# Performance work log

Measured on AMD Instinct MI355X. Metric: run time of the kernel, lower is better.

## Reference

```python
import jax, jax.numpy as jnp
import numpy as np

N_NODES = 100000
N_EDGES = 1600000
IN_CH = 128
HID = 64
OUT = 10
N_GRAPHS = 64


def gcn_conv(x, W, b, row, col, n):
    # PyG GCNConv: xw = x @ W; add self-loops (weight 1);
    # deg = scatter_add(weight, col); norm = d^-1/2[row] * d^-1/2[col];
    # out[col] += norm * xw[row]; out += b
    xw = x @ W  # [N, out_ch]
    loop = jnp.arange(n, dtype=row.dtype)
    r = jnp.concatenate([row, loop])
    c = jnp.concatenate([col, loop])
    deg = jax.ops.segment_sum(jnp.ones_like(c, dtype=xw.dtype), c, num_segments=n)
    dis = jnp.where(deg > 0, jax.lax.rsqrt(deg), 0.0)
    norm = dis[r] * dis[c]  # [E+N]
    msgs = norm[:, None] * xw[r]  # gather + scale
    agg = jax.ops.segment_sum(msgs, c, num_segments=n)  # scatter-add
    return agg + b


def global_mean_pool(x, batch, num_graphs):
    sums = jax.ops.segment_sum(x, batch, num_segments=num_graphs)
    cnt = jax.ops.segment_sum(jnp.ones((x.shape[0],), x.dtype), batch, num_segments=num_graphs)
    return sums / jnp.maximum(cnt, 1.0)[:, None]


def setup_inputs() -> dict:
    key = jax.random.key(0)
    ks = jax.random.split(key, 9)
    x = jax.random.normal(ks[0], (N_NODES, IN_CH), dtype=jnp.float32)
    edge_index = jax.random.randint(ks[1], (2, N_EDGES), 0, N_NODES, dtype=jnp.int64)
    batch = jnp.sort(jax.random.randint(ks[2], (N_NODES,), 0, N_GRAPHS, dtype=jnp.int64))
    def glorot(k, shape):
        lim = np.sqrt(6.0 / (shape[0] + shape[1]))
        return jax.random.uniform(k, shape, jnp.float32, -lim, lim)
    W1 = glorot(ks[3], (IN_CH, HID)); b1 = jnp.zeros((HID,), jnp.float32)
    W2 = glorot(ks[4], (HID, HID)); b2 = jnp.zeros((HID,), jnp.float32)
    Wl = glorot(ks[5], (HID, OUT)); bl = jnp.zeros((OUT,), jnp.float32)
    return {"x": x, "W1": W1, "b1": b1, "W2": W2, "b2": b2,
            "Wl": Wl, "bl": bl, "edge_index": edge_index, "batch": batch}


def reference(x, W1, b1, W2, b2, Wl, bl, edge_index, batch):
    row, col = edge_index[0], edge_index[1]
    n = x.shape[0]
    h = jax.nn.relu(gcn_conv(x, W1, b1, row, col, n))
    h = jax.nn.relu(gcn_conv(h, W2, b2, row, col, n))
    g = global_mean_pool(h, batch, N_GRAPHS)  # [G, HID]
    return g @ Wl + bl  # [G, OUT]
```

## Files before the change

### kernel.cpp

```cpp
#include <hip/hip_runtime.h>


static __device__ inline ushort f32_to_bf16_rne(float f) {
    uint32_t u = __float_as_uint(f);
    uint32_t r = (u + 0x7fffu + ((u >> 16) & 1u)) >> 16;
    return (ushort)r;
}

__global__ __launch_bounds__(256) void deg_kernel(const int* __restrict__ col,
                                                  int* __restrict__ deg, int E) {
    int e = blockIdx.x * 256 + threadIdx.x;
    if (e < E) atomicAdd(&deg[col[e]], 1);
}

__global__ __launch_bounds__(256) void dis_kernel(const int* __restrict__ deg,
                                                  float* __restrict__ dis, int n) {
    int i = blockIdx.x * 256 + threadIdx.x;
    if (i < n) dis[i] = rsqrtf((float)deg[i] + 1.0f);
}

__global__ __launch_bounds__(512) void block_sum_kernel(const int* __restrict__ deg,
                                                        int* __restrict__ bsums, int n) {
    __shared__ int sm[512];
    int i = blockIdx.x * 512 + threadIdx.x;
    sm[threadIdx.x] = (i < n) ? deg[i] : 0;
    __syncthreads();
    for (int s = 256; s > 0; s >>= 1) {
        if (threadIdx.x < s) sm[threadIdx.x] += sm[threadIdx.x + s];
        __syncthreads();
    }
    if (threadIdx.x == 0) bsums[blockIdx.x] = sm[0];
}

__global__ __launch_bounds__(256) void scan_bsums_kernel(int* __restrict__ bsums, int nb) {
    __shared__ int sm[256];
    int v = (threadIdx.x < nb) ? bsums[threadIdx.x] : 0;
    sm[threadIdx.x] = v;
    __syncthreads();
    for (int off = 1; off < 256; off <<= 1) {
        int t = (threadIdx.x >= off) ? sm[threadIdx.x - off] : 0;
        __syncthreads();
        sm[threadIdx.x] += t;
        __syncthreads();
    }
    if (threadIdx.x < nb) bsums[threadIdx.x] = sm[threadIdx.x] - v;
}

__global__ __launch_bounds__(512) void scan_write_kernel(const int* __restrict__ deg,
                                                         const int* __restrict__ bsums,
                                                         int* __restrict__ rowptr,
                                                         int n, int E) {
    __shared__ int sm[512];
    int i = blockIdx.x * 512 + threadIdx.x;
    int v = (i < n) ? deg[i] : 0;
    sm[threadIdx.x] = v;
    __syncthreads();
    for (int off = 1; off < 512; off <<= 1) {
        int t = (threadIdx.x >= off) ? sm[threadIdx.x - off] : 0;
        __syncthreads();
        sm[threadIdx.x] += t;
        __syncthreads();
    }
    if (i < n) rowptr[i] = bsums[blockIdx.x] + sm[threadIdx.x] - v;
    if (blockIdx.x == 0 && threadIdx.x == 0) rowptr[n] = E;
}

__global__ __launch_bounds__(256) void fill_csr_kernel(const int* __restrict__ row,
                                                       const int* __restrict__ col,
                                                       const float* __restrict__ dis,
                                                       const int* __restrict__ rowptr,
                                                       int* __restrict__ fill,
                                                       int2* __restrict__ csr, int E) {
    int e = blockIdx.x * 256 + threadIdx.x;
    if (e >= E) return;
    int r = row[e], c = col[e];
    int pos = rowptr[c] + atomicAdd(&fill[c], 1);
    csr[pos] = make_int2(r, __float_as_int(dis[r] * dis[c]));
}

template <int K>
__global__ __launch_bounds__(256) void gemm_tiled(const float* __restrict__ x,
                                                  const float* __restrict__ W,
                                                  ushort* __restrict__ out, int n) {
    __shared__ float As[32][64];
    __shared__ float Ws[32 * 64];
    const int tid = threadIdx.x;
    const int tr = tid >> 4;
    const int tc = tid & 15;
    const int base = blockIdx.x * 64;

    float acc[4][4];
#pragma unroll
    for (int i = 0; i < 4; ++i)
#pragma unroll
        for (int j = 0; j < 4; ++j) acc[i][j] = 0.0f;

    const int tnode = tid >> 3;
    const int tk4 = (tid & 7) * 4;

    for (int kc = 0; kc < K; kc += 32) {
        __syncthreads();
#pragma unroll
        for (int h = 0; h < 2; ++h) {
            int m = tnode + h * 32;
            int node = base + m;
            float4 v = make_float4(0.f, 0.f, 0.f, 0.f);
            if (node < n) v = *(const float4*)&x[(size_t)node * K + kc + tk4];
            As[tk4 + 0][m] = v.x; As[tk4 + 1][m] = v.y;
            As[tk4 + 2][m] = v.z; As[tk4 + 3][m] = v.w;
        }
#pragma unroll
        for (int r = 0; r < 2; ++r) {
            int o = tid * 4 + r * 1024;
            *(float4*)&Ws[o] = *(const float4*)&W[kc * 64 + o];
        }
        __syncthreads();
#pragma unroll
        for (int k = 0; k < 32; ++k) {
            float4 a = *(const float4*)&As[k][tr * 4];
            float4 b = *(const float4*)&Ws[k * 64 + tc * 4];
            const float av[4] = {a.x, a.y, a.z, a.w};
            const float bv[4] = {b.x, b.y, b.z, b.w};
#pragma unroll
            for (int i = 0; i < 4; ++i)
#pragma unroll
                for (int j = 0; j < 4; ++j)
                    acc[i][j] = fmaf(av[i], bv[j], acc[i][j]);
        }
    }
#pragma unroll
    for (int i = 0; i < 4; ++i) {
        int node = base + tr * 4 + i;
        if (node < n) {
            ushort4 st;
            st.x = f32_to_bf16_rne(acc[i][0]);
            st.y = f32_to_bf16_rne(acc[i][1]);
            st.z = f32_to_bf16_rne(acc[i][2]);
            st.w = f32_to_bf16_rne(acc[i][3]);
            *(ushort4*)&out[(size_t)node * 64 + tc * 4] = st;
        }
    }
}

template <int OUT_BF16>
__global__ __launch_bounds__(256) void gcn_pull_kernel(const ushort* __restrict__ xw,
                                                       const int2* __restrict__ csr,
                                                       const int* __restrict__ rowptr,
                                                       const float* __restrict__ dis,
                                                       const float* __restrict__ b,
                                                       void* __restrict__ outv, int n) {
    const int lane = threadIdx.x & 63;
    const int wid = threadIdx.x >> 6;
    const int half = lane >> 5;
    const int q = lane & 31;
    const float2 bb = ((const float2*)b)[q];

    for (int i = blockIdx.x * 4 + wid; i < n; i += gridDim.x * 4) {
        int s = rowptr[i], t = rowptr[i + 1];
        float ax = 0.0f, ay = 0.0f;
        if (half == 0) {
            float di = dis[i];
            uint32_t u = *(const uint32_t*)(xw + ((size_t)i << 6) + (q << 1));
            float w = di * di;
            ax = w * __uint_as_float(u << 16);
            ay = w * __uint_as_float(u & 0xffff0000u);
        }
        int e = s + half;
        for (; e + 2 < t; e += 4) {
            int2 p0 = csr[e];
            int2 p1 = csr[e + 2];
            uint32_t u0 = *(const uint32_t*)(xw + ((size_t)p0.x << 6) + (q << 1));
            uint32_t u1 = *(const uint32_t*)(xw + ((size_t)p1.x << 6) + (q << 1));
            float n0 = __int_as_float(p0.y), n1 = __int_as_float(p1.y);
            ax = fmaf(n0, __uint_as_float(u0 << 16), ax);
            ay = fmaf(n0, __uint_as_float(u0 & 0xffff0000u), ay);
            ax = fmaf(n1, __uint_as_float(u1 << 16), ax);
            ay = fmaf(n1, __uint_as_float(u1 & 0xffff0000u), ay);
        }
        for (; e < t; e += 2) {
            int2 p = csr[e];
            uint32_t u = *(const uint32_t*)(xw + ((size_t)p.x << 6) + (q << 1));
            float nr = __int_as_float(p.y);
            ax = fmaf(nr, __uint_as_float(u << 16), ax);
            ay = fmaf(nr, __uint_as_float(u & 0xffff0000u), ay);
        }
        ax += __shfl_xor(ax, 32);
        ay += __shfl_xor(ay, 32);
        if (half == 0) {
            float v0 = fmaxf(ax + bb.x, 0.0f);
            float v1 = fmaxf(ay + bb.y, 0.0f);
            if (OUT_BF16) {
                ushort2 st = make_ushort2(f32_to_bf16_rne(v0), f32_to_bf16_rne(v1));
                *(ushort2*)((ushort*)outv + ((size_t)i << 6) + (q << 1)) = st;
            } else {
                *(float2*)((float*)outv + ((size_t)i << 6) + (q << 1)) = make_float2(v0, v1);
            }
        }
    }
}

__global__ __launch_bounds__(256) void pool_kernel(const ushort* __restrict__ h,
                                                   const int* __restrict__ batch,
                                                   float* __restrict__ pool,
                                                   float* __restrict__ cnt, int n) {
    const int lane = threadIdx.x & 63;
    const int wid = threadIdx.x >> 6;
    const int start = (blockIdx.x * 4 + wid) * 256;
    const int end = min(start + 256, n);
    if (start >= end) return;
    int gcur = batch[start];
    float acc = 0.0f;
    int c = 0;
    for (int i = start; i < end; ++i) {
        int g = batch[i];
        if (g != gcur) {
            atomicAdd(&pool[gcur * 64 + lane], acc);
            if (lane == 0) atomicAdd(&cnt[gcur], (float)c);
            acc = 0.0f; c = 0; gcur = g;
        }
        acc += __uint_as_float((uint32_t)h[(size_t)i * 64 + lane] << 16);
        ++c;
    }
    atomicAdd(&pool[gcur * 64 + lane], acc);
    if (lane == 0) atomicAdd(&cnt[gcur], (float)c);
}

__global__ __launch_bounds__(640) void final_kernel(const float* __restrict__ pool,
                                                    const float* __restrict__ cnt,
                                                    const float* __restrict__ Wl,
                                                    const float* __restrict__ bl,
                                                    float* __restrict__ out) {
    int tid = threadIdx.x;
    int g = tid / 10, o = tid % 10;
    float inv = 1.0f / fmaxf(cnt[g], 1.0f);
    float acc = 0.0f;
#pragma unroll
    for (int l = 0; l < 64; ++l)
        acc = fmaf(pool[g * 64 + l] * inv, Wl[l * 10 + o], acc);
    out[tid] = acc + bl[o];
}

extern "C" void kernel_launch(void* const* d_in, const int* in_sizes, int n_in,
                              void* d_out, int out_size, void* d_ws, size_t ws_size,
                              hipStream_t stream) {
    const float* x  = (const float*)d_in[0];
    const float* W1 = (const float*)d_in[1];
    const float* b1 = (const float*)d_in[2];
    const float* W2 = (const float*)d_in[3];
    const float* b2 = (const float*)d_in[4];
    const float* Wl = (const float*)d_in[5];
    const float* bl = (const float*)d_in[6];
    const int*   ei = (const int*)d_in[7];
    const int*   batch = (const int*)d_in[8];
    float* out = (float*)d_out;

    const int n = in_sizes[8];
    const int E = in_sizes[7] / 2;
    const int F = 64;

    const int* row = ei;
    const int* col = ei + E;

    char* p = (char*)d_ws;
    auto alloc = [&](size_t bytes) {
        char* r = p;
        p += (bytes + 255) & ~(size_t)255;
        return r;
    };
    int*    degi   = (int*)   alloc((size_t)n * 4);
    int*    rowptr = (int*)   alloc((size_t)(n + 1) * 4);
    int*    bsums  = (int*)   alloc(256 * 4);
    float*  dis    = (float*) alloc((size_t)n * 4);
    int2*   csr    = (int2*)  alloc((size_t)E * 8);
    ushort* xwB    = (ushort*)alloc((size_t)n * F * 2);
    float*  B      = (float*) alloc((size_t)n * F * 4);
    float*  pool   = (float*) alloc(64 * 64 * 4);
    float*  cnt    = (float*) alloc(64 * 4);

    const int nb_edge = (E + 255) / 256;
    const int nb_node = (n + 255) / 256;
    const int nb_scan = (n + 511) / 512;
    const int nb_gemm = (n + 63) / 64;

    hipMemsetAsync(degi, 0, (size_t)n * 4, stream);
    deg_kernel<<<nb_edge, 256, 0, stream>>>(col, degi, E);
    block_sum_kernel<<<nb_scan, 512, 0, stream>>>(degi, bsums, n);
    scan_bsums_kernel<<<1, 256, 0, stream>>>(bsums, nb_scan);
    scan_write_kernel<<<nb_scan, 512, 0, stream>>>(degi, bsums, rowptr, n, E);
    dis_kernel<<<nb_node, 256, 0, stream>>>(degi, dis, n);
    hipMemsetAsync(degi, 0, (size_t)n * 4, stream);
    fill_csr_kernel<<<nb_edge, 256, 0, stream>>>(row, col, dis, rowptr, degi, csr, E);

    gemm_tiled<128><<<nb_gemm, 256, 0, stream>>>(x, W1, xwB, n);
    gcn_pull_kernel<0><<<2048, 256, 0, stream>>>(xwB, csr, rowptr, dis, b1, B, n);

    gemm_tiled<64><<<nb_gemm, 256, 0, stream>>>(B, W2, xwB, n);
    gcn_pull_kernel<1><<<2048, 256, 0, stream>>>(xwB, csr, rowptr, dis, b2, B, n);

    hipMemsetAsync(pool, 0, (64 * 64 + 64) * sizeof(float), stream);
    pool_kernel<<<(n + 1023) / 1024, 256, 0, stream>>>((const ushort*)B, batch, pool, cnt, n);
    final_kernel<<<1, 640, 0, stream>>>(pool, cnt, Wl, bl, out);
}
```

Measured before the change: 496.9 us.

## Fuse CSR fill with first GEMM, drop per-edge norm, fold dis into scan

Merges the dis computation into the scan-write kernel and runs the CSR fill and the first GEMM as disjoint block ranges of one launch, so the two can overlap. The CSR now stores only source indices (halving its size), and the pull kernel gathers dis[src] per edge and applies dis[dst] once at the end. The pull loop is unrolled to four edges per half-wave, and the pool kernel uses smaller chunks per wave for more parallelism. The trade is an extra random 4-byte gather per edge in exchange for less CSR traffic and fewer launches.

Measured after the change: 436.7 us. 12.1% less time.

```diff
diff --git a/kernel.cpp b/kernel.cpp
--- a/kernel.cpp
+++ b/kernel.cpp
@@ -6,17 +6,13 @@
     uint32_t r = (u + 0x7fffu + ((u >> 16) & 1u)) >> 16;
     return (ushort)r;
 }
+static __device__ inline float bf_lo(uint32_t u) { return __uint_as_float(u << 16); }
+static __device__ inline float bf_hi(uint32_t u) { return __uint_as_float(u & 0xffff0000u); }
 
 __global__ __launch_bounds__(256) void deg_kernel(const int* __restrict__ col,
                                                   int* __restrict__ deg, int E) {
     int e = blockIdx.x * 256 + threadIdx.x;
     if (e < E) atomicAdd(&deg[col[e]], 1);
-}
-
-__global__ __launch_bounds__(256) void dis_kernel(const int* __restrict__ deg,
-                                                  float* __restrict__ dis, int n) {
-    int i = blockIdx.x * 256 + threadIdx.x;
-    if (i < n) dis[i] = rsqrtf((float)deg[i] + 1.0f);
 }
 
 __global__ __launch_bounds__(512) void block_sum_kernel(const int* __restrict__ deg,
@@ -49,6 +45,7 @@
 __global__ __launch_bounds__(512) void scan_write_kernel(const int* __restrict__ deg,
                                                          const int* __restrict__ bsums,
                                                          int* __restrict__ rowptr,
+                                                         float* __restrict__ dis,
                                                          int n, int E) {
     __shared__ int sm[512];
     int i = blockIdx.x * 512 + threadIdx.x;
@@ -61,33 +58,23 @@
         sm[threadIdx.x] += t;
         __syncthreads();
     }
-    if (i < n) rowptr[i] = bsums[blockIdx.x] + sm[threadIdx.x] - v;
+    if (i < n) {
+        rowptr[i] = bsums[blockIdx.x] + sm[threadIdx.x] - v;
+        dis[i] = rsqrtf((float)v + 1.0f);
+    }
     if (blockIdx.x == 0 && threadIdx.x == 0) rowptr[n] = E;
 }
 
-__global__ __launch_bounds__(256) void fill_csr_kernel(const int* __restrict__ row,
-                                                       const int* __restrict__ col,
-                                                       const float* __restrict__ dis,
-                                                       const int* __restrict__ rowptr,
-                                                       int* __restrict__ fill,
-                                                       int2* __restrict__ csr, int E) {
-    int e = blockIdx.x * 256 + threadIdx.x;
-    if (e >= E) return;
-    int r = row[e], c = col[e];
-    int pos = rowptr[c] + atomicAdd(&fill[c], 1);
-    csr[pos] = make_int2(r, __float_as_int(dis[r] * dis[c]));
-}
-
 template <int K>
-__global__ __launch_bounds__(256) void gemm_tiled(const float* __restrict__ x,
-                                                  const float* __restrict__ W,
-                                                  ushort* __restrict__ out, int n) {
+__device__ __forceinline__ void gemm_tile_body(const float* __restrict__ x,
+                                               const float* __restrict__ W,
+                                               ushort* __restrict__ out, int n, int bx) {
     __shared__ float As[32][64];
     __shared__ float Ws[32 * 64];
     const int tid = threadIdx.x;
     const int tr = tid >> 4;
     const int tc = tid & 15;
-    const int base = blockIdx.x * 64;
+    const int base = bx * 64;
 
     float acc[4][4];
 #pragma unroll
@@ -142,9 +129,35 @@
     }
 }
 
+template <int K>
+__global__ __launch_bounds__(256) void gemm_tiled(const float* __restrict__ x,
+                                                  const float* __restrict__ W,
+                                                  ushort* __restrict__ out, int n) {
+    gemm_tile_body<K>(x, W, out, n, blockIdx.x);
+}
+
+template <int K>
+__global__ __launch_bounds__(256) void fused_fill_gemm(
+        const float* __restrict__ x, const float* __restrict__ W,
+        ushort* __restrict__ out, int n, int nb_fill,
+        const int* __restrict__ row, const int* __restrict__ col,
+        const int* __restrict__ rowptr, int* __restrict__ fill,
+        int* __restrict__ csrs, int E) {
+    if ((int)blockIdx.x >= nb_fill) {
+        gemm_tile_body<K>(x, W, out, n, blockIdx.x - nb_fill);
+        return;
+    }
+    const int stride = nb_fill * 256;
+    for (int e = blockIdx.x * 256 + threadIdx.x; e < E; e += stride) {
+        int r = row[e], c = col[e];
+        int pos = rowptr[c] + atomicAdd(&fill[c], 1);
+        csrs[pos] = r;
+    }
+}
+
 template <int OUT_BF16>
 __global__ __launch_bounds__(256) void gcn_pull_kernel(const ushort* __restrict__ xw,
-                                                       const int2* __restrict__ csr,
+                                                       const int* __restrict__ csrs,
                                                        const int* __restrict__ rowptr,
                                                        const float* __restrict__ dis,
                                                        const float* __restrict__ b,
@@ -157,38 +170,45 @@
 
     for (int i = blockIdx.x * 4 + wid; i < n; i += gridDim.x * 4) {
         int s = rowptr[i], t = rowptr[i + 1];
+        float di = dis[i];
         float ax = 0.0f, ay = 0.0f;
         if (half == 0) {
-            float di = dis[i];
             uint32_t u = *(const uint32_t*)(xw + ((size_t)i << 6) + (q << 1));
-            float w = di * di;
-            ax = w * __uint_as_float(u << 16);
-            ay = w * __uint_as_float(u & 0xffff0000u);
+            ax = di * bf_lo(u);
+            ay = di * bf_hi(u);
         }
         int e = s + half;
+        for (; e + 6 < t; e += 8) {
+            int s0 = csrs[e], s1 = csrs[e + 2], s2 = csrs[e + 4], s3 = csrs[e + 6];
+            float d0 = dis[s0], d1 = dis[s1], d2 = dis[s2], d3 = dis[s3];
+            uint32_t u0 = *(const uint32_t*)(xw + ((size_t)s0 << 6) + (q << 1));
+            uint32_t u1 = *(const uint32_t*)(xw + ((size_t)s1 << 6) + (q << 1));
+            uint32_t u2 = *(const uint32_t*)(xw + ((size_t)s2 << 6) + (q << 1));
+            uint32_t u3 = *(const uint32_t*)(xw + ((size_t)s3 << 6) + (q << 1));
+            ax = fmaf(d0, bf_lo(u0), ax); ay = fmaf(d0, bf_hi(u0), ay);
+            ax = fmaf(d1, bf_lo(u1), ax); ay = fmaf(d1, bf_hi(u1), ay);
+            ax = fmaf(d2, bf_lo(u2), ax); ay = fmaf(d2, bf_hi(u2), ay);
+            ax = fmaf(d3, bf_lo(u3), ax); ay = fmaf(d3, bf_hi(u3), ay);
+        }
         for (; e + 2 < t; e += 4) {
-            int2 p0 = csr[e];
-            int2 p1 = csr[e + 2];
-            uint32_t u0 = *(const uint32_t*)(xw + ((size_t)p0.x << 6) + (q << 1));
-            uint32_t u1 = *(const uint32_t*)(xw + ((size_t)p1.x << 6) + (q << 1));
-            float n0 = __int_as_float(p0.y), n1 = __int_as_float(p1.y);
-            ax = fmaf(n0, __uint_as_float(u0 << 16), ax);
-            ay = fmaf(n0, __uint_as_float(u0 & 0xffff0000u), ay);
-            ax = fmaf(n1, __uint_as_float(u1 << 16), ax);
-            ay = fmaf(n1, __uint_as_float(u1 & 0xffff0000u), ay);
+            int s0 = csrs[e], s1 = csrs[e + 2];
+            float d0 = dis[s0], d1 = dis[s1];
+            uint32_t u0 = *(const uint32_t*)(xw + ((size_t)s0 << 6) + (q << 1));
+            uint32_t u1 = *(const uint32_t*)(xw + ((size_t)s1 << 6) + (q << 1));
+            ax = fmaf(d0, bf_lo(u0), ax); ay = fmaf(d0, bf_hi(u0), ay);
+            ax = fmaf(d1, bf_lo(u1), ax); ay = fmaf(d1, bf_hi(u1), ay);
         }
         for (; e < t; e += 2) {
-            int2 p = csr[e];
-            uint32_t u = *(const uint32_t*)(xw + ((size_t)p.x << 6) + (q << 1));
-            float nr = __int_as_float(p.y);
-            ax = fmaf(nr, __uint_as_float(u << 16), ax);
-            ay = fmaf(nr, __uint_as_float(u & 0xffff0000u), ay);
+            int s0 = csrs[e];
+            float d0 = dis[s0];
+            uint32_t u0 = *(const uint32_t*)(xw + ((size_t)s0 << 6) + (q << 1));
+            ax = fmaf(d0, bf_lo(u0), ax); ay = fmaf(d0, bf_hi(u0), ay);
         }
         ax += __shfl_xor(ax, 32);
         ay += __shfl_xor(ay, 32);
         if (half == 0) {
-            float v0 = fmaxf(ax + bb.x, 0.0f);
-            float v1 = fmaxf(ay + bb.y, 0.0f);
+            float v0 = fmaxf(fmaf(di, ax, bb.x), 0.0f);
+            float v1 = fmaxf(fmaf(di, ay, bb.y), 0.0f);
             if (OUT_BF16) {
                 ushort2 st = make_ushort2(f32_to_bf16_rne(v0), f32_to_bf16_rne(v1));
                 *(ushort2*)((ushort*)outv + ((size_t)i << 6) + (q << 1)) = st;
@@ -205,8 +225,8 @@
                                                    float* __restrict__ cnt, int n) {
     const int lane = threadIdx.x & 63;
     const int wid = threadIdx.x >> 6;
-    const int start = (blockIdx.x * 4 + wid) * 256;
-    const int end = min(start + 256, n);
+    const int start = (blockIdx.x * 4 + wid) * 32;
+    const int end = min(start + 32, n);
     if (start >= end) return;
     int gcur = batch[start];
     float acc = 0.0f;
@@ -271,33 +291,33 @@
     int*    rowptr = (int*)   alloc((size_t)(n + 1) * 4);
     int*    bsums  = (int*)   alloc(256 * 4);
     float*  dis    = (float*) alloc((size_t)n * 4);
-    int2*   csr    = (int2*)  alloc((size_t)E * 8);
+    int*    csrs   = (int*)   alloc((size_t)E * 4);
     ushort* xwB    = (ushort*)alloc((size_t)n * F * 2);
     float*  B      = (float*) alloc((size_t)n * F * 4);
     float*  pool   = (float*) alloc(64 * 64 * 4);
     float*  cnt    = (float*) alloc(64 * 4);
 
     const int nb_edge = (E + 255) / 256;
-    const int nb_node = (n + 255) / 256;
     const int nb_scan = (n + 511) / 512;
     const int nb_gemm = (n + 63) / 64;
+    const int nb_fill = 1024;
 
     hipMemsetAsync(degi, 0, (size_t)n * 4, stream);
     deg_kernel<<<nb_edge, 256, 0, stream>>>(col, degi, E);
     block_sum_kernel<<<nb_scan, 512, 0, stream>>>(degi, bsums, n);
     scan_bsums_kernel<<<1, 256, 0, stream>>>(bsums, nb_scan);
-    scan_write_kernel<<<nb_scan, 512, 0, stream>>>(degi, bsums, rowptr, n, E);
-    dis_kernel<<<nb_node, 256, 0, stream>>>(degi, dis, n);
+    scan_write_kernel<<<nb_scan, 512, 0, stream>>>(degi, bsums, rowptr, dis, n, E);
     hipMemsetAsync(degi, 0, (size_t)n * 4, stream);
-    fill_csr_kernel<<<nb_edge, 256, 0, stream>>>(row, col, dis, rowptr, degi, csr, E);
-
-    gemm_tiled<128><<<nb_gemm, 256, 0, stream>>>(x, W1, xwB, n);
-    gcn_pull_kernel<0><<<2048, 256, 0, stream>>>(xwB, csr, rowptr, dis, b1, B, n);
+
+    fused_fill_gemm<128><<<nb_fill + nb_gemm, 256, 0, stream>>>(
+        x, W1, xwB, n, nb_fill, row, col, rowptr, degi, csrs, E);
+
+    gcn_pull_kernel<0><<<2048, 256, 0, stream>>>(xwB, csrs, rowptr, dis, b1, B, n);
 
     gemm_tiled<64><<<nb_gemm, 256, 0, stream>>>(B, W2, xwB, n);
-    gcn_pull_kernel<1><<<2048, 256, 0, stream>>>(xwB, csr, rowptr, dis, b2, B, n);
+    gcn_pull_kernel<1><<<2048, 256, 0, stream>>>(xwB, csrs, rowptr, dis, b2, B, n);
 
     hipMemsetAsync(pool, 0, (64 * 64 + 64) * sizeof(float), stream);
-    pool_kernel<<<(n + 1023) / 1024, 256, 0, stream>>>((const ushort*)B, batch, pool, cnt, n);
+    pool_kernel<<<(n + 127) / 128, 256, 0, stream>>>((const ushort*)B, batch, pool, cnt, n);
     final_kernel<<<1, 640, 0, stream>>>(pool, cnt, Wl, bl, out);
 }
```
